# Performance work log

Hardware: AMD Instinct MI355X
Metric: run time of the kernel (lower is better)

Reference implementation:

```python
import jax, jax.numpy as jnp
import numpy as np

D_MODEL = 1024
NUM_HEADS = 16
DEPTH = D_MODEL // NUM_HEADS  # 64
BATCH = 2
SEQ = 2048


def setup_inputs() -> dict:
    key = jax.random.key(0)
    ks = jax.random.split(key, 11)
    s = 0.02
    return {
        "q": jax.random.normal(ks[0], (BATCH, SEQ, D_MODEL), dtype=jnp.float32),
        "k": jax.random.normal(ks[1], (BATCH, SEQ, D_MODEL), dtype=jnp.float32),
        "v": jax.random.normal(ks[2], (BATCH, SEQ, D_MODEL), dtype=jnp.float32),
        "wq": jax.random.normal(ks[3], (D_MODEL, D_MODEL), dtype=jnp.float32) * s,
        "bq": jnp.zeros((D_MODEL,), dtype=jnp.float32),
        "wk": jax.random.normal(ks[4], (D_MODEL, D_MODEL), dtype=jnp.float32) * s,
        "bk": jnp.zeros((D_MODEL,), dtype=jnp.float32),
        "wv": jax.random.normal(ks[5], (D_MODEL, D_MODEL), dtype=jnp.float32) * s,
        "bv": jnp.zeros((D_MODEL,), dtype=jnp.float32),
        "wo": jax.random.normal(ks[6], (D_MODEL, D_MODEL), dtype=jnp.float32) * s,
        "bo": jnp.zeros((D_MODEL,), dtype=jnp.float32),
    }


def reference(q, k, v, wq, bq, wk, bk, wv, bv, wo, bo):
    B = q.shape[0]
    # QKV projections, then split heads: (B, S, H, D)
    qh = (q @ wq + bq).reshape(B, -1, NUM_HEADS, DEPTH)
    kh = (k @ wk + bk).reshape(B, -1, NUM_HEADS, DEPTH)
    vh = (v @ wv + bv).reshape(B, -1, NUM_HEADS, DEPTH)

    inv_sqrt_dk = 1.0 / jnp.sqrt(jnp.float32(DEPTH))
    # scores: (B, Lq, Lk, H)
    scores = jnp.einsum('blhd,bjhd->bljh', qh, kh) * inv_sqrt_dk
    attn = jax.nn.softmax(scores, axis=2)
    # NOTE: original code divides by sqrt(dk) a SECOND time after softmax (faithful quirk)
    attn = attn * inv_sqrt_dk
    out = jnp.einsum('bljh,bjhe->blhe', attn, vh).reshape(B, -1, NUM_HEADS * DEPTH)
    return out @ wo + bo
```

## Files before the change

### kernel.cpp

```cpp
#include <hip/hip_runtime.h>
#include <math.h>

#define D_MODEL 1024
#define NHEADS 16
#define DH 64
#define BATCH 2
#define SEQ 2048
#define M_TOTAL (BATCH * SEQ)

typedef __attribute__((ext_vector_type(8))) short bf16x8;
typedef __attribute__((ext_vector_type(4))) float f32x4;
typedef __attribute__((ext_vector_type(16))) float f32x16;
typedef __attribute__((ext_vector_type(8))) unsigned short ushort8;
typedef unsigned short u16;
typedef unsigned int u32;

#define SCALE_Q 0.18033688f

static __device__ __forceinline__ u16 f2bf(float x) {
  unsigned int u = __float_as_uint(x);
  unsigned int r = (u + 0x7fffu + ((u >> 16) & 1u)) >> 16;
  return (u16)r;
}
static __device__ __forceinline__ u32 pk2bf(float a, float b) {
  return (u32)f2bf(a) | ((u32)f2bf(b) << 16);
}
static __device__ __forceinline__ u32 pkhu(float a, float b) {
  return __builtin_amdgcn_perm(__float_as_uint(b) + 0x8000u,
                               __float_as_uint(a) + 0x8000u, 0x07060302u);
}
static __device__ __forceinline__ float exp2fast(float x) {
  return __builtin_amdgcn_exp2f(x);
}

static __device__ __forceinline__ void gl_lds16(const u16* g, u16* l) {
  __builtin_amdgcn_global_load_lds(
      (const __attribute__((address_space(1))) u32*)g,
      (__attribute__((address_space(3))) u32*)l, 16, 0, 0);
}

__global__ __launch_bounds__(256) void prep_kernel(
    const float* __restrict__ q, const float* __restrict__ k, const float* __restrict__ v,
    u16* __restrict__ qb, u16* __restrict__ kb, u16* __restrict__ vb,
    const float* __restrict__ w0, const float* __restrict__ w1,
    const float* __restrict__ w2, const float* __restrict__ w3,
    u16* __restrict__ t0, u16* __restrict__ t1,
    u16* __restrict__ t2, u16* __restrict__ t3) {
  __shared__ float tf[64 * 68];
  const int z = blockIdx.z;
  const int tid = threadIdx.x;
  if (z < 3) {
    const float* src = (z == 0) ? q : (z == 1) ? k : v;
    u16* dst = (z == 0) ? qb : (z == 1) ? kb : vb;
    const size_t i = ((size_t)blockIdx.x * 256 + tid) * 8;
    float4 a = *reinterpret_cast<const float4*>(src + i);
    float4 b = *reinterpret_cast<const float4*>(src + i + 4);
    u32 o0 = pk2bf(a.x, a.y), o1 = pk2bf(a.z, a.w);
    u32 o2 = pk2bf(b.x, b.y), o3 = pk2bf(b.z, b.w);
    *reinterpret_cast<uint4*>(dst + i) = make_uint4(o0, o1, o2, o3);
    return;
  }
  if (blockIdx.x >= 256) return;
  const int zz = z - 3;
  const float* w = (zz == 0) ? w0 : (zz == 1) ? w1 : (zz == 2) ? w2 : w3;
  u16* wt = (zz == 0) ? t0 : (zz == 1) ? t1 : (zz == 2) ? t2 : t3;
  const int n0 = (blockIdx.x & 15) * 64, k0 = (blockIdx.x >> 4) * 64;
  const int kl = tid >> 4, nq = (tid & 15) * 4;
#pragma unroll
  for (int c = 0; c < 4; ++c) {
    float4 vv = *reinterpret_cast<const float4*>(
        &w[(size_t)(k0 + kl + c * 16) * 1024 + n0 + nq]);
    *reinterpret_cast<float4*>(&tf[(kl + c * 16) * 68 + nq]) = vv;
  }
  __syncthreads();
  const int n = tid & 63, kq = tid >> 6;
  u32 pk[8];
#pragma unroll
  for (int p = 0; p < 8; ++p) {
    float a = tf[(kq * 16 + 2 * p) * 68 + n];
    float b = tf[(kq * 16 + 2 * p + 1) * 68 + n];
    pk[p] = pk2bf(a, b);
  }
  u16* dst = &wt[(size_t)(n0 + n) * 1024 + k0 + kq * 16];
  *reinterpret_cast<uint4*>(dst) = make_uint4(pk[0], pk[1], pk[2], pk[3]);
  *reinterpret_cast<uint4*>(dst + 8) = make_uint4(pk[4], pk[5], pk[6], pk[7]);
}

__global__ __launch_bounds__(256) void qkv_gemm_kernel(
    const u16* __restrict__ qb, const u16* __restrict__ kb, const u16* __restrict__ vb,
    const u16* __restrict__ wqT, const u16* __restrict__ wkT, const u16* __restrict__ wvT,
    const float* __restrict__ bq, const float* __restrict__ bk, const float* __restrict__ bv,
    u16* __restrict__ qh, u16* __restrict__ kh, u16* __restrict__ vhT) {
  __shared__ u16 lds[9216];
  u16* sA = lds;
  u16* sB = lds + 4096;

  const int z = blockIdx.z;
  const u16* A  = (z == 0) ? qb : (z == 1) ? kb : vb;
  const u16* BT = (z == 0) ? wqT : (z == 1) ? wkT : wvT;
  const float* bias = (z == 0) ? bq : (z == 1) ? bk : bv;

  int wg = blockIdx.x + 8 * blockIdx.y;
  wg = (wg & 7) * 32 + (wg >> 3);
  const int m0 = (wg >> 3) * 128;
  const int n0 = (wg & 7) * 128;

  const int tid = threadIdx.x;
  const int w = tid >> 6, l = tid & 63;
  const int wr = w >> 1, wc = w & 1;
  const int n = l & 15, g = l >> 4;

  const u16* Ab = A + (size_t)(m0 + w * 16 + (l >> 2)) * 1024 + (l & 3) * 8;
  const u16* Bb = BT + (size_t)(n0 + w * 16 + (l >> 2)) * 1024 + (l & 3) * 8;
  u16* sAb = sA + w * 512;
  u16* sBb = sB + w * 512;

  f32x4 acc[4][4];
#pragma unroll
  for (int fm = 0; fm < 4; ++fm)
#pragma unroll
    for (int fn = 0; fn < 4; ++fn) acc[fm][fn] = (f32x4)(0.0f);

  for (int kk = 0; kk < 1024; kk += 32) {
    __syncthreads();
    gl_lds16(Ab + kk, sAb);
    gl_lds16(Ab + kk + (size_t)64 * 1024, sAb + 2048);
    gl_lds16(Bb + kk, sBb);
    gl_lds16(Bb + kk + (size_t)64 * 1024, sBb + 2048);
    __syncthreads();
    bf16x8 af[4], bf[4];
#pragma unroll
    for (int f = 0; f < 4; ++f)
      af[f] = *reinterpret_cast<const bf16x8*>(&sA[(wr * 64 + f * 16 + n) * 32 + g * 8]);
#pragma unroll
    for (int f = 0; f < 4; ++f)
      bf[f] = *reinterpret_cast<const bf16x8*>(&sB[(wc * 64 + f * 16 + n) * 32 + g * 8]);
#pragma unroll
    for (int fm = 0; fm < 4; ++fm)
#pragma unroll
      for (int fn = 0; fn < 4; ++fn)
        acc[fm][fn] = __builtin_amdgcn_mfma_f32_16x16x32_bf16(af[fm], bf[fn], acc[fm][fn], 0, 0, 0);
  }

  float bv4[4];
#pragma unroll
  for (int fn = 0; fn < 4; ++fn) bv4[fn] = bias[n0 + wc * 64 + fn * 16 + n];

  if (z < 2) {
    const float scale = (z == 0) ? SCALE_Q : 1.0f;
    u16* dst = (z == 0) ? qh : kh;
#pragma unroll
    for (int fm = 0; fm < 4; ++fm)
#pragma unroll
      for (int fn = 0; fn < 4; ++fn)
#pragma unroll
        for (int rr = 0; rr < 4; ++rr) {
          const int row = m0 + wr * 64 + fm * 16 + g * 4 + rr;
          const int col = n0 + wc * 64 + fn * 16 + n;
          dst[(size_t)row * 1024 + col] = f2bf((acc[fm][fn][rr] + bv4[fn]) * scale);
        }
  } else {
    __syncthreads();
    u16* bw = lds + w * 2304;
    const int hh = (n0 >> 6) + wc;
    const int bb = m0 >> 11;
    const int c = l >> 1, half = l & 1;
    const int sbase = (m0 & 2047) + wr * 64 + half * 32;
#pragma unroll
    for (int p = 0; p < 2; ++p) {
#pragma unroll
      for (int fh = 0; fh < 2; ++fh) {
        const int fn = p * 2 + fh;
#pragma unroll
        for (int fm = 0; fm < 4; ++fm)
#pragma unroll
          for (int rr = 0; rr < 4; ++rr)
            bw[(fh * 16 + n) * 72 + fm * 16 + g * 4 + rr] =
                f2bf(acc[fm][fn][rr] + bv4[fn]);
      }
      __syncthreads();
      u16* gd = vhT + ((size_t)((bb * NHEADS + hh) * DH + p * 32 + c)) * SEQ + sbase;
#pragma unroll
      for (int j = 0; j < 4; ++j)
        *reinterpret_cast<uint4*>(gd + j * 8) =
            *reinterpret_cast<const uint4*>(&bw[c * 72 + half * 32 + j * 8]);
      __syncthreads();
    }
  }
}

__global__ __launch_bounds__(256) void out_gemm_kernel(
    const u16* __restrict__ aob, const u16* __restrict__ woT,
    const float* __restrict__ bo, float* __restrict__ out) {
  __shared__ u16 lds[6144];
  u16* sA = lds;
  u16* sB = lds + 4096;

  int wg = blockIdx.x + 16 * blockIdx.y;
  wg = (wg & 7) * 64 + (wg >> 3);
  const int m0 = (wg >> 4) * 128;
  const int n0 = (wg & 15) * 64;

  const int tid = threadIdx.x;
  const int w = tid >> 6, l = tid & 63;
  const int wr = w >> 1, wc = w & 1;
  const int n = l & 15, g = l >> 4;

  const u16* Ab = aob + (size_t)(m0 + w * 16 + (l >> 2)) * 1024 + (l & 3) * 8;
  const u16* Bb = woT + (size_t)(n0 + w * 16 + (l >> 2)) * 1024 + (l & 3) * 8;
  u16* sAb = sA + w * 512;
  u16* sBb = sB + w * 512;

  f32x4 acc[4][2];
#pragma unroll
  for (int fm = 0; fm < 4; ++fm)
#pragma unroll
    for (int fn = 0; fn < 2; ++fn) acc[fm][fn] = (f32x4)(0.0f);

  for (int kk = 0; kk < 1024; kk += 32) {
    __syncthreads();
    gl_lds16(Ab + kk, sAb);
    gl_lds16(Ab + kk + (size_t)64 * 1024, sAb + 2048);
    gl_lds16(Bb + kk, sBb);
    __syncthreads();
    bf16x8 af[4], bf[2];
#pragma unroll
    for (int f = 0; f < 4; ++f)
      af[f] = *reinterpret_cast<const bf16x8*>(&sA[(wr * 64 + f * 16 + n) * 32 + g * 8]);
#pragma unroll
    for (int f = 0; f < 2; ++f)
      bf[f] = *reinterpret_cast<const bf16x8*>(&sB[(wc * 32 + f * 16 + n) * 32 + g * 8]);
#pragma unroll
    for (int fm = 0; fm < 4; ++fm)
#pragma unroll
      for (int fn = 0; fn < 2; ++fn)
        acc[fm][fn] = __builtin_amdgcn_mfma_f32_16x16x32_bf16(af[fm], bf[fn], acc[fm][fn], 0, 0, 0);
  }

  const float b0 = bo[n0 + wc * 32 + n];
  const float b1 = bo[n0 + wc * 32 + 16 + n];
#pragma unroll
  for (int fm = 0; fm < 4; ++fm)
#pragma unroll
    for (int rr = 0; rr < 4; ++rr) {
      const int row = m0 + wr * 64 + fm * 16 + g * 4 + rr;
      out[(size_t)row * 1024 + n0 + wc * 32 + n] = acc[fm][0][rr] + b0;
      out[(size_t)row * 1024 + n0 + wc * 32 + 16 + n] = acc[fm][1][rr] + b1;
    }
}

#define KT 64
__global__ __launch_bounds__(256, 2) void attn_mfma_kernel(
    const u16* __restrict__ qh, const u16* __restrict__ kh,
    const u16* __restrict__ vhT, u16* __restrict__ aob) {
  const int bid = blockIdx.x;
  const int xcd = bid & 7;
  const int idx = bid >> 3;
  const int bh = (xcd << 2) | (idx >> 4);
  const int qt = idx & 15;
  const int b = bh >> 4, h = bh & 15;

  const int tid = threadIdx.x;
  const int w = tid >> 6, l = tid & 63;
  const int lr = l & 31;
  const int g1 = l >> 5;
  const int q0 = qt * 128 + w * 32;

  __shared__ u16 Ks[2][KT * DH];
  __shared__ u16 Vs[2][DH * KT];

  union { u32 u[4]; bf16x8 v; } onesu;
  onesu.u[0] = onesu.u[1] = onesu.u[2] = onesu.u[3] = 0x3F803F80u;

  bf16x8 qf[4];
#pragma unroll
  for (int kq = 0; kq < 4; ++kq)
    qf[kq] = *reinterpret_cast<const bf16x8*>(
        &qh[((size_t)(b * SEQ + q0 + lr)) * D_MODEL + h * DH + kq * 16 + g1 * 8]);

  f32x16 O0 = (f32x16)(0.0f), O1 = (f32x16)(0.0f), L0 = (f32x16)(0.0f);

  const int srow = tid >> 2, sq = tid & 3;
  const u16* kp0 = kh + (size_t)(b * SEQ + srow) * D_MODEL + h * DH + sq * 16;
  const u16* vp0 = vhT + ((size_t)((b * NHEADS + h) * DH + srow)) * SEQ + sq * 16;
  const int sbase = srow * 64 + sq * 16;
  const int sxor = (srow & 7) << 3;
  const int rxor = (lr & 7) << 3;

  ushort8 kr[2], vr[2];
#pragma unroll
  for (int c = 0; c < 2; ++c) {
    kr[c] = *reinterpret_cast<const ushort8*>(kp0 + c * 8);
    vr[c] = *reinterpret_cast<const ushort8*>(vp0 + c * 8);
  }
#pragma unroll
  for (int c = 0; c < 2; ++c) {
    const int sidx = (sbase + c * 8) ^ sxor;
    *reinterpret_cast<ushort8*>(&Ks[0][sidx]) = kr[c];
    *reinterpret_cast<ushort8*>(&Vs[0][sidx]) = vr[c];
  }
  __syncthreads();

  int cur = 0;
  for (int jt = 0; jt < SEQ / KT; ++jt) {
    if (jt + 1 < SEQ / KT) {
      const int off = (jt + 1) * KT;
#pragma unroll
      for (int c = 0; c < 2; ++c) {
        kr[c] = *reinterpret_cast<const ushort8*>(kp0 + (size_t)off * D_MODEL + c * 8);
        vr[c] = *reinterpret_cast<const ushort8*>(vp0 + off + c * 8);
      }
    }

    __builtin_amdgcn_s_setprio(1);
    f32x16 St0 = (f32x16)(0.0f), St1 = (f32x16)(0.0f);
#pragma unroll
    for (int kq = 0; kq < 4; ++kq) {
      const int coff = kq * 16 + g1 * 8;
      bf16x8 kf0 = *reinterpret_cast<const bf16x8*>(&Ks[cur][(lr * 64 + coff) ^ rxor]);
      bf16x8 kf1 = *reinterpret_cast<const bf16x8*>(&Ks[cur][((32 + lr) * 64 + coff) ^ rxor]);
      St0 = __builtin_amdgcn_mfma_f32_32x32x16_bf16(kf0, qf[kq], St0, 0, 0, 0);
      St1 = __builtin_amdgcn_mfma_f32_32x32x16_bf16(kf1, qf[kq], St1, 0, 0, 0);
    }
    __builtin_amdgcn_s_setprio(0);

    u32 U0[8], U1[8];
#pragma unroll
    for (int s = 0; s < 8; ++s) {
      float a0 = exp2fast(St0[2 * s]), b0 = exp2fast(St0[2 * s + 1]);
      float a1 = exp2fast(St1[2 * s]), b1 = exp2fast(St1[2 * s + 1]);
      U0[s] = pkhu(a0, b0);
      U1[s] = pkhu(a1, b1);
    }

    __builtin_amdgcn_s_setprio(1);
#pragma unroll
    for (int kb2 = 0; kb2 < 2; ++kb2) {
#pragma unroll
      for (int m16 = 0; m16 < 2; ++m16) {
        union { u32 u[4]; bf16x8 v; } pa;
        if (kb2 == 0) {
          pa.u[0] = U0[m16 * 4 + 0]; pa.u[1] = U0[m16 * 4 + 1];
          pa.u[2] = U0[m16 * 4 + 2]; pa.u[3] = U0[m16 * 4 + 3];
        } else {
          pa.u[0] = U1[m16 * 4 + 0]; pa.u[1] = U1[m16 * 4 + 1];
          pa.u[2] = U1[m16 * 4 + 2]; pa.u[3] = U1[m16 * 4 + 3];
        }
        const int koff = kb2 * 32 + m16 * 16 + g1 * 4;
        union { u32 u[4]; bf16x8 v; } vb0, vb1;
        *reinterpret_cast<uint2*>(&vb0.u[0]) =
            *reinterpret_cast<const uint2*>(&Vs[cur][(lr * 64 + koff) ^ rxor]);
        *reinterpret_cast<uint2*>(&vb0.u[2]) =
            *reinterpret_cast<const uint2*>(&Vs[cur][(lr * 64 + koff + 8) ^ rxor]);
        *reinterpret_cast<uint2*>(&vb1.u[0]) =
            *reinterpret_cast<const uint2*>(&Vs[cur][((32 + lr) * 64 + koff) ^ rxor]);
        *reinterpret_cast<uint2*>(&vb1.u[2]) =
            *reinterpret_cast<const uint2*>(&Vs[cur][((32 + lr) * 64 + koff + 8) ^ rxor]);
        O0 = __builtin_amdgcn_mfma_f32_32x32x16_bf16(pa.v, vb0.v, O0, 0, 0, 0);
        O1 = __builtin_amdgcn_mfma_f32_32x32x16_bf16(pa.v, vb1.v, O1, 0, 0, 0);
        L0 = __builtin_amdgcn_mfma_f32_32x32x16_bf16(pa.v, onesu.v, L0, 0, 0, 0);
      }
    }
    __builtin_amdgcn_s_setprio(0);

    if (jt + 1 < SEQ / KT) {
#pragma unroll
      for (int c = 0; c < 2; ++c) {
        const int sidx = (sbase + c * 8) ^ sxor;
        *reinterpret_cast<ushort8*>(&Ks[cur ^ 1][sidx]) = kr[c];
        *reinterpret_cast<ushort8*>(&Vs[cur ^ 1][sidx]) = vr[c];
      }
    }
    __syncthreads();
    cur ^= 1;
  }

  float invr[16];
#pragma unroll
  for (int r = 0; r < 16; ++r) invr[r] = 0.125f / L0[r];
#pragma unroll
  for (int dblk = 0; dblk < 2; ++dblk) {
#pragma unroll
    for (int s = 0; s < 8; ++s) {
      const int r0 = 2 * s, r1 = 2 * s + 1;
      float x0 = (dblk ? O1[r0] : O0[r0]) * invr[r0];
      float x1 = (dblk ? O1[r1] : O0[r1]) * invr[r1];
      const int row0 = q0 + (r0 & 3) + 8 * (r0 >> 2) + 4 * g1;
      const int row1 = q0 + (r1 & 3) + 8 * (r1 >> 2) + 4 * g1;
      const int col = h * DH + dblk * 32 + lr;
      aob[((size_t)(b * SEQ + row0)) * D_MODEL + col] = f2bf(x0);
      aob[((size_t)(b * SEQ + row1)) * D_MODEL + col] = f2bf(x1);
    }
  }
}

extern "C" void kernel_launch(void* const* d_in, const int* in_sizes, int n_in,
                              void* d_out, int out_size, void* d_ws, size_t ws_size,
                              hipStream_t stream) {
  const float* q  = (const float*)d_in[0];
  const float* k  = (const float*)d_in[1];
  const float* v  = (const float*)d_in[2];
  const float* wq = (const float*)d_in[3];
  const float* bq = (const float*)d_in[4];
  const float* wk = (const float*)d_in[5];
  const float* bk = (const float*)d_in[6];
  const float* wv = (const float*)d_in[7];
  const float* bv = (const float*)d_in[8];
  const float* wo = (const float*)d_in[9];
  const float* bo = (const float*)d_in[10];
  float* out = (float*)d_out;

  const size_t wcount = (size_t)D_MODEL * D_MODEL;
  const size_t tcount = (size_t)M_TOTAL * D_MODEL;
  u16* wqT = (u16*)d_ws;
  u16* wkT = wqT + wcount;
  u16* wvT = wkT + wcount;
  u16* woT = wvT + wcount;
  u16* qb  = woT + wcount;
  u16* kb  = qb + tcount;
  u16* vb  = kb + tcount;
  u16* qh  = vb + tcount;
  u16* kh  = qh + tcount;
  u16* vhT = kh + tcount;
  u16* aob = qb;

  dim3 blk(256);

  prep_kernel<<<dim3(2048, 1, 7), blk, 0, stream>>>(
      q, k, v, qb, kb, vb, wq, wk, wv, wo, wqT, wkT, wvT, woT);

  qkv_gemm_kernel<<<dim3(8, 32, 3), blk, 0, stream>>>(
      qb, kb, vb, wqT, wkT, wvT, bq, bk, bv, qh, kh, vhT);

  attn_mfma_kernel<<<dim3(512), blk, 0, stream>>>(qh, kh, vhT, aob);

  out_gemm_kernel<<<dim3(16, 32), blk, 0, stream>>>(aob, woT, bo, out);
}
```

Measured before the change: 133.5 us.

## Double-buffer LDS tiles in QKV and output projection GEMMs

Both projection GEMM kernels now use two LDS stages. The next K-slice is prefetched with the async global-to-LDS loads before the MFMA work on the current slice, replacing the two barriers per iteration with one at the end. The aim is to hide global load latency behind the matrix math. The cost is a larger shared memory footprint per block (32 KB and 24 KB), which can lower the number of resident blocks per CU.

```diff
diff --git a/kernel.cpp b/kernel.cpp
--- a/kernel.cpp
+++ b/kernel.cpp
@@ -91,9 +91,7 @@
     const u16* __restrict__ wqT, const u16* __restrict__ wkT, const u16* __restrict__ wvT,
     const float* __restrict__ bq, const float* __restrict__ bk, const float* __restrict__ bv,
     u16* __restrict__ qh, u16* __restrict__ kh, u16* __restrict__ vhT) {
-  __shared__ u16 lds[9216];
-  u16* sA = lds;
-  u16* sB = lds + 4096;
+  __shared__ u16 lds[16384];
 
   const int z = blockIdx.z;
   const u16* A  = (z == 0) ? qb : (z == 1) ? kb : vb;
@@ -112,8 +110,7 @@
 
   const u16* Ab = A + (size_t)(m0 + w * 16 + (l >> 2)) * 1024 + (l & 3) * 8;
   const u16* Bb = BT + (size_t)(n0 + w * 16 + (l >> 2)) * 1024 + (l & 3) * 8;
-  u16* sAb = sA + w * 512;
-  u16* sBb = sB + w * 512;
+  const int wb = w * 512;
 
   f32x4 acc[4][4];
 #pragma unroll
@@ -121,25 +118,38 @@
 #pragma unroll
     for (int fn = 0; fn < 4; ++fn) acc[fm][fn] = (f32x4)(0.0f);
 
+  gl_lds16(Ab, lds + wb);
+  gl_lds16(Ab + (size_t)64 * 1024, lds + wb + 2048);
+  gl_lds16(Bb, lds + 8192 + wb);
+  gl_lds16(Bb + (size_t)64 * 1024, lds + 8192 + wb + 2048);
+  __syncthreads();
+
+  int cur = 0;
   for (int kk = 0; kk < 1024; kk += 32) {
-    __syncthreads();
-    gl_lds16(Ab + kk, sAb);
-    gl_lds16(Ab + kk + (size_t)64 * 1024, sAb + 2048);
-    gl_lds16(Bb + kk, sBb);
-    gl_lds16(Bb + kk + (size_t)64 * 1024, sBb + 2048);
-    __syncthreads();
+    u16* sAc = lds + cur * 4096;
+    u16* sBc = lds + 8192 + cur * 4096;
+    if (kk + 32 < 1024) {
+      u16* sAn = lds + (cur ^ 1) * 4096;
+      u16* sBn = lds + 8192 + (cur ^ 1) * 4096;
+      gl_lds16(Ab + kk + 32, sAn + wb);
+      gl_lds16(Ab + kk + 32 + (size_t)64 * 1024, sAn + wb + 2048);
+      gl_lds16(Bb + kk + 32, sBn + wb);
+      gl_lds16(Bb + kk + 32 + (size_t)64 * 1024, sBn + wb + 2048);
+    }
     bf16x8 af[4], bf[4];
 #pragma unroll
     for (int f = 0; f < 4; ++f)
-      af[f] = *reinterpret_cast<const bf16x8*>(&sA[(wr * 64 + f * 16 + n) * 32 + g * 8]);
+      af[f] = *reinterpret_cast<const bf16x8*>(&sAc[(wr * 64 + f * 16 + n) * 32 + g * 8]);
 #pragma unroll
     for (int f = 0; f < 4; ++f)
-      bf[f] = *reinterpret_cast<const bf16x8*>(&sB[(wc * 64 + f * 16 + n) * 32 + g * 8]);
+      bf[f] = *reinterpret_cast<const bf16x8*>(&sBc[(wc * 64 + f * 16 + n) * 32 + g * 8]);
 #pragma unroll
     for (int fm = 0; fm < 4; ++fm)
 #pragma unroll
       for (int fn = 0; fn < 4; ++fn)
         acc[fm][fn] = __builtin_amdgcn_mfma_f32_16x16x32_bf16(af[fm], bf[fn], acc[fm][fn], 0, 0, 0);
+    __syncthreads();
+    cur ^= 1;
   }
 
   float bv4[4];
@@ -192,9 +202,7 @@
 __global__ __launch_bounds__(256) void out_gemm_kernel(
     const u16* __restrict__ aob, const u16* __restrict__ woT,
     const float* __restrict__ bo, float* __restrict__ out) {
-  __shared__ u16 lds[6144];
-  u16* sA = lds;
-  u16* sB = lds + 4096;
+  __shared__ u16 lds[12288];
 
   int wg = blockIdx.x + 16 * blockIdx.y;
   wg = (wg & 7) * 64 + (wg >> 3);
@@ -208,8 +216,7 @@
 
   const u16* Ab = aob + (size_t)(m0 + w * 16 + (l >> 2)) * 1024 + (l & 3) * 8;
   const u16* Bb = woT + (size_t)(n0 + w * 16 + (l >> 2)) * 1024 + (l & 3) * 8;
-  u16* sAb = sA + w * 512;
-  u16* sBb = sB + w * 512;
+  const int wb = w * 512;
 
   f32x4 acc[4][2];
 #pragma unroll
@@ -217,24 +224,36 @@
 #pragma unroll
     for (int fn = 0; fn < 2; ++fn) acc[fm][fn] = (f32x4)(0.0f);
 
+  gl_lds16(Ab, lds + wb);
+  gl_lds16(Ab + (size_t)64 * 1024, lds + wb + 2048);
+  gl_lds16(Bb, lds + 8192 + wb);
+  __syncthreads();
+
+  int cur = 0;
   for (int kk = 0; kk < 1024; kk += 32) {
-    __syncthreads();
-    gl_lds16(Ab + kk, sAb);
-    gl_lds16(Ab + kk + (size_t)64 * 1024, sAb + 2048);
-    gl_lds16(Bb + kk, sBb);
-    __syncthreads();
+    u16* sAc = lds + cur * 4096;
+    u16* sBc = lds + 8192 + cur * 2048;
+    if (kk + 32 < 1024) {
+      u16* sAn = lds + (cur ^ 1) * 4096;
+      u16* sBn = lds + 8192 + (cur ^ 1) * 2048;
+      gl_lds16(Ab + kk + 32, sAn + wb);
+      gl_lds16(Ab + kk + 32 + (size_t)64 * 1024, sAn + wb + 2048);
+      gl_lds16(Bb + kk + 32, sBn + wb);
+    }
     bf16x8 af[4], bf[2];
 #pragma unroll
     for (int f = 0; f < 4; ++f)
-      af[f] = *reinterpret_cast<const bf16x8*>(&sA[(wr * 64 + f * 16 + n) * 32 + g * 8]);
+      af[f] = *reinterpret_cast<const bf16x8*>(&sAc[(wr * 64 + f * 16 + n) * 32 + g * 8]);
 #pragma unroll
     for (int f = 0; f < 2; ++f)
-      bf[f] = *reinterpret_cast<const bf16x8*>(&sB[(wc * 32 + f * 16 + n) * 32 + g * 8]);
+      bf[f] = *reinterpret_cast<const bf16x8*>(&sBc[(wc * 32 + f * 16 + n) * 32 + g * 8]);
 #pragma unroll
     for (int fm = 0; fm < 4; ++fm)
 #pragma unroll
       for (int fn = 0; fn < 2; ++fn)
         acc[fm][fn] = __builtin_amdgcn_mfma_f32_16x16x32_bf16(af[fm], bf[fn], acc[fm][fn], 0, 0, 0);
+    __syncthreads();
+    cur ^= 1;
   }
 
   const float b0 = bo[n0 + wc * 32 + n];
```

New measurement: 118.9 us, median of 2. -10.9%, faster.
